# Kernel tuning notes

Measured on AMD Instinct MI355X. Metric: run time of the kernel, lower is better.

## Reference

```python
import jax, jax.numpy as jnp
import numpy as np

B, T, C = 4, 2048, 1024
N_HEAD = 16
HEAD_DIM = C // N_HEAD
SCALE = 1.0 / np.sqrt(HEAD_DIM).astype(np.float32)


def setup_inputs() -> dict:
    key = jax.random.key(0)
    k1, k2, k3 = jax.random.split(key, 3)
    x = jax.random.normal(k1, (B, T, C), dtype=jnp.float32)
    # torch Linear weights: [out_features, in_features], scaled init
    w_qkv = jax.random.normal(k2, (3 * C, C), dtype=jnp.float32) * (1.0 / np.sqrt(C))
    w_out = jax.random.normal(k3, (C, C), dtype=jnp.float32) * (1.0 / np.sqrt(C))
    b_out = jnp.zeros((C,), dtype=jnp.float32)
    return {"x": x, "w_qkv": w_qkv, "w_out": w_out, "b_out": b_out}


def reference(x, w_qkv, w_out, b_out):
    Bsz, Tlen, Cdim = x.shape
    qkv = jnp.einsum('btc,oc->bto', x, w_qkv)  # [B,T,3C]
    q, k, v = jnp.split(qkv, 3, axis=-1)
    # [B,H,T,D]
    def heads(t):
        return t.reshape(Bsz, Tlen, N_HEAD, HEAD_DIM).transpose(0, 2, 1, 3)
    q, k, v = heads(q), heads(k), heads(v)
    att = jnp.einsum('bhqd,bhkd->bhqk', q, k) * SCALE  # [B,H,T,T]
    causal = jnp.tril(jnp.ones((Tlen, Tlen), dtype=bool))
    att = jnp.where(causal[None, None], att, -jnp.inf)
    att = jax.nn.softmax(att, axis=-1)
    out = jnp.einsum('bhqk,bhkd->bhqd', att, v)
    out = out.transpose(0, 2, 1, 3).reshape(Bsz, Tlen, Cdim)
    out = jnp.einsum('btc,oc->bto', out, w_out) + b_out
    return out
```

## Files before the change

kernel.cpp:

```cpp
#include <hip/hip_runtime.h>
#include <stdint.h>


typedef __attribute__((ext_vector_type(8))) short bf16x8;
typedef __attribute__((ext_vector_type(4))) float f32x4;

#define EXP2F(x) __builtin_amdgcn_exp2f(x)
#define SL2E 0.18033688011112042f
#define FIXED_M 15.0f

template <bool B> struct BoolC { static constexpr bool value = B; };
template <int I> struct IntC { static constexpr int value = I; };

__device__ __forceinline__ short f2bf(float f) {
  union { float f; unsigned u; } c; c.f = f;
  unsigned u = c.u;
  unsigned r = (u + 0x7fffu + ((u >> 16) & 1u)) >> 16;
  return (short)(unsigned short)r;
}

__device__ __forceinline__ void softmax_pack(const f32x4* sc, bf16x8& pa0, bf16x8& pa1) {
  union U { int i[4]; bf16x8 v; };
  U u0, u1;
#pragma unroll
  for (int j = 0; j < 4; ++j) {
    float p0 = EXP2F(sc[j][0]);
    float p1 = EXP2F(sc[j][1]);
    float p2 = EXP2F(sc[j][2]);
    float p3 = EXP2F(sc[j][3]);
    int w0, w1;
    asm("v_cvt_pk_bf16_f32 %0, %1, %2" : "=v"(w0) : "v"(p0), "v"(p1));
    asm("v_cvt_pk_bf16_f32 %0, %1, %2" : "=v"(w1) : "v"(p2), "v"(p3));
    if (j < 2) { u0.i[j * 2] = w0; u0.i[j * 2 + 1] = w1; }
    else       { u1.i[(j - 2) * 2] = w0; u1.i[(j - 2) * 2 + 1] = w1; }
  }
  pa0 = u0.v;
  pa1 = u1.v;
}

__device__ __forceinline__ void llds16(const short* g, short* l) {
  __builtin_amdgcn_global_load_lds(
      (const __attribute__((address_space(1))) unsigned int*)g,
      (__attribute__((address_space(3))) unsigned int*)l, 16, 0, 0);
}

__global__ __launch_bounds__(256) void cast_all(
    const float* __restrict__ x, const float* __restrict__ wq,
    const float* __restrict__ wo, short* __restrict__ xb,
    short* __restrict__ wqb, short* __restrict__ wob) {
  const int b = blockIdx.x;
  const float* src;
  short* dst;
  int idx;
  if (b < 8192)        { src = x;  dst = xb;  idx = b * 256 + threadIdx.x; }
  else if (b < 11264)  { src = wq; dst = wqb; idx = (b - 8192) * 256 + threadIdx.x; }
  else                 { src = wo; dst = wob; idx = (b - 11264) * 256 + threadIdx.x; }
  float4 f = ((const float4*)src)[idx];
  short4 o;
  o.x = f2bf(f.x); o.y = f2bf(f.y); o.z = f2bf(f.z); o.w = f2bf(f.w);
  ((short4*)dst)[idx] = o;
}

__global__ __launch_bounds__(512) void gemm_qkv(
    const short* __restrict__ A, const short* __restrict__ Bw,
    short* __restrict__ Qo, short* __restrict__ Ko, short* __restrict__ Vt) {
  const int K = 1024;
  __shared__ short smem[49152];
  const int tid = threadIdx.x;
  const int lane = tid & 63;
  const int wave = tid >> 6;
  const int wr = wave >> 1;
  const int wc = wave & 1;
  const int m0 = blockIdx.y * 256;
  const int n0 = blockIdx.x * 128;
  const int mrow = lane & 15;
  const int kq = lane >> 4;

  f32x4 acc[4][4];
#pragma unroll
  for (int i = 0; i < 4; ++i)
#pragma unroll
    for (int j = 0; j < 4; ++j) acc[i][j] = (f32x4){0.f, 0.f, 0.f, 0.f};

  auto stageA = [&](int t, int buf, int ca) {
    const int c = ca * 512 + tid;
    const int row = c >> 3;
    const int sc = (c & 7) ^ (row & 7);
    llds16(A + (size_t)(m0 + row) * K + t * 64 + sc * 8,
           &smem[buf * 24576 + c * 8]);
  };
  auto stageB = [&](int t, int buf, int cb) {
    const int c = cb * 512 + tid;
    const int row = c >> 3;
    const int sc = (c & 7) ^ (row & 7);
    llds16(Bw + (size_t)(n0 + row) * K + t * 64 + sc * 8,
           &smem[buf * 24576 + 16384 + c * 8]);
  };

  auto rdA = [&](const short* lA, int i, int kk) -> bf16x8 {
    const int row = wr * 64 + i * 16 + mrow;
    const int ch = (kq + 4 * kk) ^ (row & 7);
    return *(const bf16x8*)&lA[row * 64 + ch * 8];
  };
  auto rdB = [&](const short* lB, int j, int kk) -> bf16x8 {
    const int row = wc * 64 + j * 16 + mrow;
    const int ch = (kq + 4 * kk) ^ (row & 7);
    return *(const bf16x8*)&lB[row * 64 + ch * 8];
  };

  stageA(0, 0, 0); stageA(0, 0, 1); stageA(0, 0, 2); stageA(0, 0, 3);
  stageB(0, 0, 0); stageB(0, 0, 1);
  asm volatile("s_waitcnt vmcnt(0)" ::: "memory");
  __syncthreads();

#define PHASE_TAIL()                                         \
  __builtin_amdgcn_s_barrier();                              \
  asm volatile("s_waitcnt lgkmcnt(0)" ::: "memory");         \
  __builtin_amdgcn_sched_barrier(0);                         \
  __builtin_amdgcn_s_setprio(1);

#define PHASE_END()                                          \
  __builtin_amdgcn_s_setprio(0);                             \
  __builtin_amdgcn_sched_barrier(0);                         \
  __builtin_amdgcn_s_barrier();

  for (int t = 0; t < 16; ++t) {
    const int buf = t & 1;
    const int nb = buf ^ 1;
    const short* lA = &smem[buf * 24576];
    const short* lB = lA + 16384;
    bf16x8 a0, a1, a2, a3, bf0, bf1, bf2, bf3;

    a0 = rdA(lA, 0, 0); a1 = rdA(lA, 1, 0);
    bf0 = rdB(lB, 0, 0); bf1 = rdB(lB, 1, 0);
    bf2 = rdB(lB, 2, 0); bf3 = rdB(lB, 3, 0);
    if (t < 15) { stageA(t + 1, nb, 0); stageA(t + 1, nb, 1); }
    PHASE_TAIL();
    acc[0][0] = __builtin_amdgcn_mfma_f32_16x16x32_bf16(a0, bf0, acc[0][0], 0, 0, 0);
    acc[0][1] = __builtin_amdgcn_mfma_f32_16x16x32_bf16(a0, bf1, acc[0][1], 0, 0, 0);
    acc[0][2] = __builtin_amdgcn_mfma_f32_16x16x32_bf16(a0, bf2, acc[0][2], 0, 0, 0);
    acc[0][3] = __builtin_amdgcn_mfma_f32_16x16x32_bf16(a0, bf3, acc[0][3], 0, 0, 0);
    acc[1][0] = __builtin_amdgcn_mfma_f32_16x16x32_bf16(a1, bf0, acc[1][0], 0, 0, 0);
    acc[1][1] = __builtin_amdgcn_mfma_f32_16x16x32_bf16(a1, bf1, acc[1][1], 0, 0, 0);
    acc[1][2] = __builtin_amdgcn_mfma_f32_16x16x32_bf16(a1, bf2, acc[1][2], 0, 0, 0);
    acc[1][3] = __builtin_amdgcn_mfma_f32_16x16x32_bf16(a1, bf3, acc[1][3], 0, 0, 0);
    PHASE_END();

    a2 = rdA(lA, 2, 0); a3 = rdA(lA, 3, 0);
    if (t < 15) { stageA(t + 1, nb, 2); stageA(t + 1, nb, 3); }
    PHASE_TAIL();
    acc[2][0] = __builtin_amdgcn_mfma_f32_16x16x32_bf16(a2, bf0, acc[2][0], 0, 0, 0);
    acc[2][1] = __builtin_amdgcn_mfma_f32_16x16x32_bf16(a2, bf1, acc[2][1], 0, 0, 0);
    acc[2][2] = __builtin_amdgcn_mfma_f32_16x16x32_bf16(a2, bf2, acc[2][2], 0, 0, 0);
    acc[2][3] = __builtin_amdgcn_mfma_f32_16x16x32_bf16(a2, bf3, acc[2][3], 0, 0, 0);
    acc[3][0] = __builtin_amdgcn_mfma_f32_16x16x32_bf16(a3, bf0, acc[3][0], 0, 0, 0);
    acc[3][1] = __builtin_amdgcn_mfma_f32_16x16x32_bf16(a3, bf1, acc[3][1], 0, 0, 0);
    acc[3][2] = __builtin_amdgcn_mfma_f32_16x16x32_bf16(a3, bf2, acc[3][2], 0, 0, 0);
    acc[3][3] = __builtin_amdgcn_mfma_f32_16x16x32_bf16(a3, bf3, acc[3][3], 0, 0, 0);
    PHASE_END();

    a0 = rdA(lA, 0, 1); a1 = rdA(lA, 1, 1);
    bf0 = rdB(lB, 0, 1); bf1 = rdB(lB, 1, 1);
    bf2 = rdB(lB, 2, 1); bf3 = rdB(lB, 3, 1);
    if (t < 15) { stageB(t + 1, nb, 0); stageB(t + 1, nb, 1); }
    PHASE_TAIL();
    acc[0][0] = __builtin_amdgcn_mfma_f32_16x16x32_bf16(a0, bf0, acc[0][0], 0, 0, 0);
    acc[0][1] = __builtin_amdgcn_mfma_f32_16x16x32_bf16(a0, bf1, acc[0][1], 0, 0, 0);
    acc[0][2] = __builtin_amdgcn_mfma_f32_16x16x32_bf16(a0, bf2, acc[0][2], 0, 0, 0);
    acc[0][3] = __builtin_amdgcn_mfma_f32_16x16x32_bf16(a0, bf3, acc[0][3], 0, 0, 0);
    acc[1][0] = __builtin_amdgcn_mfma_f32_16x16x32_bf16(a1, bf0, acc[1][0], 0, 0, 0);
    acc[1][1] = __builtin_amdgcn_mfma_f32_16x16x32_bf16(a1, bf1, acc[1][1], 0, 0, 0);
    acc[1][2] = __builtin_amdgcn_mfma_f32_16x16x32_bf16(a1, bf2, acc[1][2], 0, 0, 0);
    acc[1][3] = __builtin_amdgcn_mfma_f32_16x16x32_bf16(a1, bf3, acc[1][3], 0, 0, 0);
    PHASE_END();

    a2 = rdA(lA, 2, 1); a3 = rdA(lA, 3, 1);
    PHASE_TAIL();
    acc[2][0] = __builtin_amdgcn_mfma_f32_16x16x32_bf16(a2, bf0, acc[2][0], 0, 0, 0);
    acc[2][1] = __builtin_amdgcn_mfma_f32_16x16x32_bf16(a2, bf1, acc[2][1], 0, 0, 0);
    acc[2][2] = __builtin_amdgcn_mfma_f32_16x16x32_bf16(a2, bf2, acc[2][2], 0, 0, 0);
    acc[2][3] = __builtin_amdgcn_mfma_f32_16x16x32_bf16(a2, bf3, acc[2][3], 0, 0, 0);
    acc[3][0] = __builtin_amdgcn_mfma_f32_16x16x32_bf16(a3, bf0, acc[3][0], 0, 0, 0);
    acc[3][1] = __builtin_amdgcn_mfma_f32_16x16x32_bf16(a3, bf1, acc[3][1], 0, 0, 0);
    acc[3][2] = __builtin_amdgcn_mfma_f32_16x16x32_bf16(a3, bf2, acc[3][2], 0, 0, 0);
    acc[3][3] = __builtin_amdgcn_mfma_f32_16x16x32_bf16(a3, bf3, acc[3][3], 0, 0, 0);
    __builtin_amdgcn_s_setprio(0);
    __builtin_amdgcn_sched_barrier(0);
    if (t < 15) asm volatile("s_waitcnt vmcnt(0)" ::: "memory");
    __builtin_amdgcn_s_barrier();
  }
#undef PHASE_TAIL
#undef PHASE_END

  __syncthreads();

  const int b = m0 >> 11;
  if (n0 < 2048) {
    const float sc_ = ((n0 >> 10) == 1) ? SL2E : 1.0f;
    short* lC = smem;
#pragma unroll
    for (int i = 0; i < 4; ++i) {
      const int rl = wr * 64 + i * 16 + kq * 4;
#pragma unroll
      for (int j = 0; j < 4; ++j) {
        const int col = wc * 64 + j * 16 + mrow;
#pragma unroll
        for (int r = 0; r < 4; ++r)
          lC[(rl + r) * 132 + col] = f2bf(acc[i][j][r] * sc_);
      }
    }
    __syncthreads();
    short* dst = (n0 >> 10) == 0 ? Qo : Ko;
#pragma unroll
    for (int call = 0; call < 8; ++call) {
      const int cc = call * 512 + tid;
      const int row = cc >> 4;
      const int ch = cc & 15;
      const int t = (m0 & 2047) + row;
      const int c = (n0 + ch * 8) & 1023;
      const int h = c >> 6;
      const int d = c & 63;
      bf16x8 val = *(const bf16x8*)&lC[row * 132 + ch * 8];
      *(bf16x8*)(dst + ((size_t)(b * 16 + h) * 2048 + t) * 64 + d) = val;
    }
  } else {
    short* lCt = smem;
#pragma unroll
    for (int i = 0; i < 4; ++i) {
      const int rl = wr * 64 + i * 16 + kq * 4;
#pragma unroll
      for (int j = 0; j < 4; ++j) {
        const int col = wc * 64 + j * 16 + mrow;
#pragma unroll
        for (int r = 0; r < 4; ++r)
          lCt[col * 264 + rl + r] = f2bf(acc[i][j][r]);
      }
    }
    __syncthreads();
#pragma unroll
    for (int call = 0; call < 8; ++call) {
      const int cc = call * 512 + tid;
      const int col = cc >> 5;
      const int tg = cc & 31;
      const int o = n0 + col;
      const int d = o & 63;
      const int h = (o >> 6) & 15;
      const int t = (m0 & 2047) + tg * 8;
      bf16x8 val = *(const bf16x8*)&lCt[col * 264 + tg * 8];
      *(bf16x8*)(Vt + ((size_t)(b * 16 + h) * 64 + d) * 2048 + t) = val;
    }
  }
}

__global__ __launch_bounds__(256) void gemm_out(
    const short* __restrict__ A, const short* __restrict__ Bw,
    const float* __restrict__ bias, float* __restrict__ Out) {
  const int K = 1024;
  __shared__ short smem[16384];
  const int tid = threadIdx.x;
  const int lane = tid & 63;
  const int wave = tid >> 6;
  const int m0 = blockIdx.y * 128;
  const int n0 = blockIdx.x * 128;
  const int wm = (wave >> 1) * 64;
  const int wn = (wave & 1) * 64;
  const int mrow = lane & 15;
  const int kq = lane >> 4;

  f32x4 acc[4][4];
#pragma unroll
  for (int i = 0; i < 4; ++i)
#pragma unroll
    for (int j = 0; j < 4; ++j) acc[i][j] = (f32x4){0.f, 0.f, 0.f, 0.f};

  auto stage = [&](int it, int buf) {
#pragma unroll
    for (int call = 0; call < 2; ++call) {
      const int cb = call * 256 + wave * 64;
      const int c = cb + lane;
      const int row = c >> 2;
      const int scol = (c & 3) ^ ((row ^ (row >> 2)) & 3);
      llds16(A + (size_t)(m0 + row) * K + it * 32 + scol * 8,
             &smem[buf * 8192 + cb * 8]);
      llds16(Bw + (size_t)(n0 + row) * K + it * 32 + scol * 8,
             &smem[buf * 8192 + 4096 + cb * 8]);
    }
  };

  stage(0, 0);
  __syncthreads();

  for (int it = 0; it < 32; ++it) {
    const int buf = it & 1;
    if (it < 31) stage(it + 1, buf ^ 1);
    const short* lA = &smem[buf * 8192];
    const short* lB = &smem[buf * 8192 + 4096];
    bf16x8 af[4], bfr[4];
#pragma unroll
    for (int i = 0; i < 4; ++i) {
      const int row = wm + i * 16 + mrow;
      af[i] = *(const bf16x8*)&lA[row * 32 + (((kq ^ row ^ (row >> 2)) & 3) * 8)];
    }
#pragma unroll
    for (int j = 0; j < 4; ++j) {
      const int row = wn + j * 16 + mrow;
      bfr[j] = *(const bf16x8*)&lB[row * 32 + (((kq ^ row ^ (row >> 2)) & 3) * 8)];
    }
#pragma unroll
    for (int i = 0; i < 4; ++i)
#pragma unroll
      for (int j = 0; j < 4; ++j)
        acc[i][j] = __builtin_amdgcn_mfma_f32_16x16x32_bf16(af[i], bfr[j], acc[i][j], 0, 0, 0);
    __syncthreads();
  }

#pragma unroll
  for (int i = 0; i < 4; ++i) {
    const int m = m0 + wm + i * 16 + kq * 4;
#pragma unroll
    for (int j = 0; j < 4; ++j) {
      const int n = n0 + wn + j * 16 + mrow;
      const float bb = bias[n];
#pragma unroll
      for (int r = 0; r < 4; ++r)
        Out[(size_t)(m + r) * 1024 + n] = acc[i][j][r] + bb;
    }
  }
}

__global__ __launch_bounds__(256) void flash_attn(
    const short* __restrict__ Qg, const short* __restrict__ Kg,
    const short* __restrict__ Vtg, short* __restrict__ Og) {
  const int T = 2048;
  __shared__ short lK[2][64 * 64];
  __shared__ short lVt[2][64 * 64];
  const int tid = threadIdx.x;
  const int lane = tid & 63;
  const int wave = tid >> 6;
  const int bh = blockIdx.x;
  const int bx = blockIdx.y;
  const int mrow = lane & 15;
  const int kq = lane >> 4;
  const int swz = mrow & 7;
  const size_t base = (size_t)bh * T * 64;
  const size_t vbase = (size_t)bh * 64 * T;

  int qts[4];
  qts[0] = bx;
  qts[1] = 31 - bx;
  qts[2] = 15 - bx;
  qts[3] = 16 + bx;

  const bf16x8 ones = {0x3F80, 0x3F80, 0x3F80, 0x3F80, 0x3F80, 0x3F80, 0x3F80, 0x3F80};

  bf16x8 aq0[4], aq1[4];
#pragma unroll
  for (int s = 0; s < 4; ++s) {
    const short* qp = Qg + base + (size_t)(qts[s] * 64 + wave * 16 + mrow) * 64 + kq * 8;
    aq0[s] = *(const bf16x8*)qp;
    aq1[s] = *(const bf16x8*)(qp + 32);
  }

  f32x4 acc[4][4], lac[4];
#pragma unroll
  for (int s = 0; s < 4; ++s) {
    lac[s] = (f32x4){0.f, 0.f, 0.f, 0.f};
#pragma unroll
    for (int jd = 0; jd < 4; ++jd) acc[s][jd] = (f32x4){0.f, 0.f, 0.f, 0.f};
  }

  auto stage = [&](int nt, int buf) {
#pragma unroll
    for (int call = 0; call < 2; ++call) {
      const int cb = call * 256 + wave * 64;
      const int c = cb + lane;
      const int row = c >> 3;
      const int scol = (c & 7) ^ (row & 7);
      const int grow = (row & 0x23) | ((row & 0x0C) << 1) | ((row & 0x10) >> 2);
      llds16(Kg + base + (size_t)(nt * 64 + grow) * 64 + scol * 8, &lK[buf][cb * 8]);
      llds16(Vtg + vbase + (size_t)row * T + nt * 64 + scol * 8, &lVt[buf][cb * 8]);
    }
  };

  auto seg = [&](auto Aa, auto Pi, const short* K_, const short* Vt_, int kt) {
    constexpr bool ACT0 = decltype(Aa)::value;
    constexpr int pi = decltype(Pi)::value;
    f32x4 sc0[4], sc1[4];
#pragma unroll
    for (int j = 0; j < 4; ++j) {
      const short* krow = &K_[(j * 16 + mrow) * 64];
      bf16x8 kb0 = *(const bf16x8*)&krow[(kq ^ swz) * 8];
      bf16x8 kb1 = *(const bf16x8*)&krow[((4 + kq) ^ swz) * 8];
      __builtin_amdgcn_s_setprio(1);
      f32x4 ss = (f32x4){-FIXED_M, -FIXED_M, -FIXED_M, -FIXED_M};
      ss = __builtin_amdgcn_mfma_f32_16x16x32_bf16(kb0, aq0[pi + 1], ss, 0, 0, 0);
      ss = __builtin_amdgcn_mfma_f32_16x16x32_bf16(kb1, aq1[pi + 1], ss, 0, 0, 0);
      sc1[j] = ss;
      if constexpr (ACT0) {
        f32x4 s2 = (f32x4){-FIXED_M, -FIXED_M, -FIXED_M, -FIXED_M};
        s2 = __builtin_amdgcn_mfma_f32_16x16x32_bf16(kb0, aq0[pi], s2, 0, 0, 0);
        s2 = __builtin_amdgcn_mfma_f32_16x16x32_bf16(kb1, aq1[pi], s2, 0, 0, 0);
        sc0[j] = s2;
      }
      __builtin_amdgcn_s_setprio(0);
    }

    if (kt == qts[pi + 1]) {
      const int qcol = qts[pi + 1] * 64 + wave * 16 + mrow;
#pragma unroll
      for (int j = 0; j < 4; ++j) {
        const int keyb = kt * 64 + ((j & 2) << 4) + (kq << 3) + ((j & 1) << 2);
#pragma unroll
        for (int r = 0; r < 4; ++r)
          if (keyb + r > qcol) sc1[j][r] = -1e30f;
      }
    }
    if constexpr (ACT0) {
      if (kt == qts[pi]) {
        const int qcol = qts[pi] * 64 + wave * 16 + mrow;
#pragma unroll
        for (int j = 0; j < 4; ++j) {
          const int keyb = kt * 64 + ((j & 2) << 4) + (kq << 3) + ((j & 1) << 2);
#pragma unroll
          for (int r = 0; r < 4; ++r)
            if (keyb + r > qcol) sc0[j][r] = -1e30f;
        }
      }
    }

    bf16x8 pa0_1, pa1_1, pa0_0, pa1_0;
    softmax_pack(sc1, pa0_1, pa1_1);
    lac[pi + 1] = __builtin_amdgcn_mfma_f32_16x16x32_bf16(pa0_1, ones, lac[pi + 1], 0, 0, 0);
    lac[pi + 1] = __builtin_amdgcn_mfma_f32_16x16x32_bf16(pa1_1, ones, lac[pi + 1], 0, 0, 0);
    if constexpr (ACT0) {
      softmax_pack(sc0, pa0_0, pa1_0);
      lac[pi] = __builtin_amdgcn_mfma_f32_16x16x32_bf16(pa0_0, ones, lac[pi], 0, 0, 0);
      lac[pi] = __builtin_amdgcn_mfma_f32_16x16x32_bf16(pa1_0, ones, lac[pi], 0, 0, 0);
    }

#pragma unroll
    for (int jd = 0; jd < 4; ++jd) {
      const short* vrow = &Vt_[(jd * 16 + mrow) * 64];
      bf16x8 vb0 = *(const bf16x8*)&vrow[(kq ^ swz) * 8];
      bf16x8 vb1 = *(const bf16x8*)&vrow[((4 + kq) ^ swz) * 8];
      __builtin_amdgcn_s_setprio(1);
      acc[pi + 1][jd] = __builtin_amdgcn_mfma_f32_16x16x32_bf16(pa0_1, vb0, acc[pi + 1][jd], 0, 0, 0);
      acc[pi + 1][jd] = __builtin_amdgcn_mfma_f32_16x16x32_bf16(pa1_1, vb1, acc[pi + 1][jd], 0, 0, 0);
      if constexpr (ACT0) {
        acc[pi][jd] = __builtin_amdgcn_mfma_f32_16x16x32_bf16(pa0_0, vb0, acc[pi][jd], 0, 0, 0);
        acc[pi][jd] = __builtin_amdgcn_mfma_f32_16x16x32_bf16(pa1_0, vb1, acc[pi][jd], 0, 0, 0);
      }
      __builtin_amdgcn_s_setprio(0);
    }
  };

  stage(0, 0);
  const int ktmax = qts[1];
  for (int kt = 0; kt <= ktmax; ++kt) {
    const int bcur = kt & 1;
    if (kt < ktmax) {
      stage(kt + 1, bcur ^ 1);
      asm volatile("s_waitcnt vmcnt(4)" ::: "memory");
    } else {
      asm volatile("s_waitcnt vmcnt(0)" ::: "memory");
    }
    __builtin_amdgcn_s_barrier();
    const short* K_ = lK[bcur];
    const short* Vt_ = lVt[bcur];
    if (kt <= qts[0]) seg(BoolC<true>{}, IntC<0>{}, K_, Vt_, kt);
    else              seg(BoolC<false>{}, IntC<0>{}, K_, Vt_, kt);
    if (kt <= qts[3]) {
      if (kt <= qts[2]) seg(BoolC<true>{}, IntC<1 * 2>{}, K_, Vt_, kt);
      else              seg(BoolC<false>{}, IntC<1 * 2>{}, K_, Vt_, kt);
    }
    __builtin_amdgcn_s_barrier();
  }

  const int b = bh >> 4;
  const int h = bh & 15;
#pragma unroll
  for (int s = 0; s < 4; ++s) {
#pragma unroll
    for (int r = 0; r < 4; ++r) {
      const float inv = 1.0f / lac[s][r];
      const int t = qts[s] * 64 + wave * 16 + kq * 4 + r;
#pragma unroll
      for (int jd = 0; jd < 4; ++jd) {
        const int col = h * 64 + jd * 16 + mrow;
        Og[((size_t)b * 2048 + t) * 1024 + col] = f2bf(acc[s][jd][r] * inv);
      }
    }
  }
}

extern "C" void kernel_launch(void* const* d_in, const int* in_sizes, int n_in,
                              void* d_out, int out_size, void* d_ws, size_t ws_size,
                              hipStream_t stream) {
  const float* x = (const float*)d_in[0];
  const float* w_qkv = (const float*)d_in[1];
  const float* w_out = (const float*)d_in[2];
  const float* b_out = (const float*)d_in[3];
  float* out = (float*)d_out;

  char* ws = (char*)d_ws;
  const size_t NX = 8192ull * 1024;
  const size_t NWQ = 3072ull * 1024;
  const size_t NWO = 1024ull * 1024;
  const size_t NQ = 64ull * 2048 * 64;
  size_t off = 0;
  short* xb    = (short*)(ws + off); off += NX * 2;
  short* wqkvb = (short*)(ws + off); off += NWQ * 2;
  short* woutb = (short*)(ws + off); off += NWO * 2;
  short* q     = (short*)(ws + off); off += NQ * 2;
  short* k     = (short*)(ws + off); off += NQ * 2;
  short* vt    = (short*)(ws + off); off += NQ * 2;
  short* attb  = (short*)(ws + off); off += NX * 2;
  if (off > ws_size) return;

  cast_all<<<12288, 256, 0, stream>>>(x, w_qkv, w_out, xb, wqkvb, woutb);
  gemm_qkv<<<dim3(24, 32), 512, 0, stream>>>(xb, wqkvb, q, k, vt);
  flash_attn<<<dim3(64, 8), 256, 0, stream>>>(q, k, vt, attb);
  gemm_out<<<dim3(8, 64), 256, 0, stream>>>(attb, woutb, b_out, out);
}
```

Before: 248.2 us.

## Restructure output GEMM into 256x128 tiles with phased MFMA/load interleaving

The output projection GEMM now runs 512-thread blocks on 256x128 tiles with a K-step of 64. Each step splits into four phases that interleave LDS fragment reads, async global-to-LDS staging of the next tile, and MFMA bursts, with explicit barriers, waitcnts and setprio. The goal is to hide global load latency behind matrix math and get more reuse per tile. In exchange it uses more LDS (96KB) and more barriers per step, and halves the block count, which may hurt occupancy or tail balance.

```diff
diff --git a/kernel.cpp b/kernel.cpp
--- a/kernel.cpp
+++ b/kernel.cpp
@@ -252,18 +252,18 @@
   }
 }
 
-__global__ __launch_bounds__(256) void gemm_out(
+__global__ __launch_bounds__(512) void gemm_out(
     const short* __restrict__ A, const short* __restrict__ Bw,
     const float* __restrict__ bias, float* __restrict__ Out) {
   const int K = 1024;
-  __shared__ short smem[16384];
+  __shared__ short smem[49152];
   const int tid = threadIdx.x;
   const int lane = tid & 63;
   const int wave = tid >> 6;
-  const int m0 = blockIdx.y * 128;
+  const int wr = wave >> 1;
+  const int wc = wave & 1;
+  const int m0 = blockIdx.y * 256;
   const int n0 = blockIdx.x * 128;
-  const int wm = (wave >> 1) * 64;
-  const int wn = (wave & 1) * 64;
   const int mrow = lane & 15;
   const int kq = lane >> 4;
 
@@ -273,53 +273,122 @@
 #pragma unroll
     for (int j = 0; j < 4; ++j) acc[i][j] = (f32x4){0.f, 0.f, 0.f, 0.f};
 
-  auto stage = [&](int it, int buf) {
-#pragma unroll
-    for (int call = 0; call < 2; ++call) {
-      const int cb = call * 256 + wave * 64;
-      const int c = cb + lane;
-      const int row = c >> 2;
-      const int scol = (c & 3) ^ ((row ^ (row >> 2)) & 3);
-      llds16(A + (size_t)(m0 + row) * K + it * 32 + scol * 8,
-             &smem[buf * 8192 + cb * 8]);
-      llds16(Bw + (size_t)(n0 + row) * K + it * 32 + scol * 8,
-             &smem[buf * 8192 + 4096 + cb * 8]);
-    }
-  };
-
-  stage(0, 0);
+  auto stageA = [&](int t, int buf, int ca) {
+    const int c = ca * 512 + tid;
+    const int row = c >> 3;
+    const int sc = (c & 7) ^ (row & 7);
+    llds16(A + (size_t)(m0 + row) * K + t * 64 + sc * 8,
+           &smem[buf * 24576 + c * 8]);
+  };
+  auto stageB = [&](int t, int buf, int cb) {
+    const int c = cb * 512 + tid;
+    const int row = c >> 3;
+    const int sc = (c & 7) ^ (row & 7);
+    llds16(Bw + (size_t)(n0 + row) * K + t * 64 + sc * 8,
+           &smem[buf * 24576 + 16384 + c * 8]);
+  };
+
+  auto rdA = [&](const short* lA, int i, int kk) -> bf16x8 {
+    const int row = wr * 64 + i * 16 + mrow;
+    const int ch = (kq + 4 * kk) ^ (row & 7);
+    return *(const bf16x8*)&lA[row * 64 + ch * 8];
+  };
+  auto rdB = [&](const short* lB, int j, int kk) -> bf16x8 {
+    const int row = wc * 64 + j * 16 + mrow;
+    const int ch = (kq + 4 * kk) ^ (row & 7);
+    return *(const bf16x8*)&lB[row * 64 + ch * 8];
+  };
+
+  stageA(0, 0, 0); stageA(0, 0, 1); stageA(0, 0, 2); stageA(0, 0, 3);
+  stageB(0, 0, 0); stageB(0, 0, 1);
+  asm volatile("s_waitcnt vmcnt(0)" ::: "memory");
   __syncthreads();
 
-  for (int it = 0; it < 32; ++it) {
-    const int buf = it & 1;
-    if (it < 31) stage(it + 1, buf ^ 1);
-    const short* lA = &smem[buf * 8192];
-    const short* lB = &smem[buf * 8192 + 4096];
-    bf16x8 af[4], bfr[4];
-#pragma unroll
-    for (int i = 0; i < 4; ++i) {
-      const int row = wm + i * 16 + mrow;
-      af[i] = *(const bf16x8*)&lA[row * 32 + (((kq ^ row ^ (row >> 2)) & 3) * 8)];
-    }
+#define PHASE_TAIL()                                         \
+  __builtin_amdgcn_s_barrier();                              \
+  asm volatile("s_waitcnt lgkmcnt(0)" ::: "memory");         \
+  __builtin_amdgcn_sched_barrier(0);                         \
+  __builtin_amdgcn_s_setprio(1);
+
+#define PHASE_END()                                          \
+  __builtin_amdgcn_s_setprio(0);                             \
+  __builtin_amdgcn_sched_barrier(0);                         \
+  __builtin_amdgcn_s_barrier();
+
+  for (int t = 0; t < 16; ++t) {
+    const int buf = t & 1;
+    const int nb = buf ^ 1;
+    const short* lA = &smem[buf * 24576];
+    const short* lB = lA + 16384;
+    bf16x8 a0, a1, a2, a3, bf0, bf1, bf2, bf3;
+
+    a0 = rdA(lA, 0, 0); a1 = rdA(lA, 1, 0);
+    bf0 = rdB(lB, 0, 0); bf1 = rdB(lB, 1, 0);
+    bf2 = rdB(lB, 2, 0); bf3 = rdB(lB, 3, 0);
+    if (t < 15) { stageA(t + 1, nb, 0); stageA(t + 1, nb, 1); }
+    PHASE_TAIL();
+    acc[0][0] = __builtin_amdgcn_mfma_f32_16x16x32_bf16(a0, bf0, acc[0][0], 0, 0, 0);
+    acc[0][1] = __builtin_amdgcn_mfma_f32_16x16x32_bf16(a0, bf1, acc[0][1], 0, 0, 0);
+    acc[0][2] = __builtin_amdgcn_mfma_f32_16x16x32_bf16(a0, bf2, acc[0][2], 0, 0, 0);
+    acc[0][3] = __builtin_amdgcn_mfma_f32_16x16x32_bf16(a0, bf3, acc[0][3], 0, 0, 0);
+    acc[1][0] = __builtin_amdgcn_mfma_f32_16x16x32_bf16(a1, bf0, acc[1][0], 0, 0, 0);
+    acc[1][1] = __builtin_amdgcn_mfma_f32_16x16x32_bf16(a1, bf1, acc[1][1], 0, 0, 0);
+    acc[1][2] = __builtin_amdgcn_mfma_f32_16x16x32_bf16(a1, bf2, acc[1][2], 0, 0, 0);
+    acc[1][3] = __builtin_amdgcn_mfma_f32_16x16x32_bf16(a1, bf3, acc[1][3], 0, 0, 0);
+    PHASE_END();
+
+    a2 = rdA(lA, 2, 0); a3 = rdA(lA, 3, 0);
+    if (t < 15) { stageA(t + 1, nb, 2); stageA(t + 1, nb, 3); }
+    PHASE_TAIL();
+    acc[2][0] = __builtin_amdgcn_mfma_f32_16x16x32_bf16(a2, bf0, acc[2][0], 0, 0, 0);
+    acc[2][1] = __builtin_amdgcn_mfma_f32_16x16x32_bf16(a2, bf1, acc[2][1], 0, 0, 0);
+    acc[2][2] = __builtin_amdgcn_mfma_f32_16x16x32_bf16(a2, bf2, acc[2][2], 0, 0, 0);
+    acc[2][3] = __builtin_amdgcn_mfma_f32_16x16x32_bf16(a2, bf3, acc[2][3], 0, 0, 0);
+    acc[3][0] = __builtin_amdgcn_mfma_f32_16x16x32_bf16(a3, bf0, acc[3][0], 0, 0, 0);
+    acc[3][1] = __builtin_amdgcn_mfma_f32_16x16x32_bf16(a3, bf1, acc[3][1], 0, 0, 0);
+    acc[3][2] = __builtin_amdgcn_mfma_f32_16x16x32_bf16(a3, bf2, acc[3][2], 0, 0, 0);
+    acc[3][3] = __builtin_amdgcn_mfma_f32_16x16x32_bf16(a3, bf3, acc[3][3], 0, 0, 0);
+    PHASE_END();
+
+    a0 = rdA(lA, 0, 1); a1 = rdA(lA, 1, 1);
+    bf0 = rdB(lB, 0, 1); bf1 = rdB(lB, 1, 1);
+    bf2 = rdB(lB, 2, 1); bf3 = rdB(lB, 3, 1);
+    if (t < 15) { stageB(t + 1, nb, 0); stageB(t + 1, nb, 1); }
+    PHASE_TAIL();
+    acc[0][0] = __builtin_amdgcn_mfma_f32_16x16x32_bf16(a0, bf0, acc[0][0], 0, 0, 0);
+    acc[0][1] = __builtin_amdgcn_mfma_f32_16x16x32_bf16(a0, bf1, acc[0][1], 0, 0, 0);
+    acc[0][2] = __builtin_amdgcn_mfma_f32_16x16x32_bf16(a0, bf2, acc[0][2], 0, 0, 0);
+    acc[0][3] = __builtin_amdgcn_mfma_f32_16x16x32_bf16(a0, bf3, acc[0][3], 0, 0, 0);
+    acc[1][0] = __builtin_amdgcn_mfma_f32_16x16x32_bf16(a1, bf0, acc[1][0], 0, 0, 0);
+    acc[1][1] = __builtin_amdgcn_mfma_f32_16x16x32_bf16(a1, bf1, acc[1][1], 0, 0, 0);
+    acc[1][2] = __builtin_amdgcn_mfma_f32_16x16x32_bf16(a1, bf2, acc[1][2], 0, 0, 0);
+    acc[1][3] = __builtin_amdgcn_mfma_f32_16x16x32_bf16(a1, bf3, acc[1][3], 0, 0, 0);
+    PHASE_END();
+
+    a2 = rdA(lA, 2, 1); a3 = rdA(lA, 3, 1);
+    PHASE_TAIL();
+    acc[2][0] = __builtin_amdgcn_mfma_f32_16x16x32_bf16(a2, bf0, acc[2][0], 0, 0, 0);
+    acc[2][1] = __builtin_amdgcn_mfma_f32_16x16x32_bf16(a2, bf1, acc[2][1], 0, 0, 0);
+    acc[2][2] = __builtin_amdgcn_mfma_f32_16x16x32_bf16(a2, bf2, acc[2][2], 0, 0, 0);
+    acc[2][3] = __builtin_amdgcn_mfma_f32_16x16x32_bf16(a2, bf3, acc[2][3], 0, 0, 0);
+    acc[3][0] = __builtin_amdgcn_mfma_f32_16x16x32_bf16(a3, bf0, acc[3][0], 0, 0, 0);
+    acc[3][1] = __builtin_amdgcn_mfma_f32_16x16x32_bf16(a3, bf1, acc[3][1], 0, 0, 0);
+    acc[3][2] = __builtin_amdgcn_mfma_f32_16x16x32_bf16(a3, bf2, acc[3][2], 0, 0, 0);
+    acc[3][3] = __builtin_amdgcn_mfma_f32_16x16x32_bf16(a3, bf3, acc[3][3], 0, 0, 0);
+    __builtin_amdgcn_s_setprio(0);
+    __builtin_amdgcn_sched_barrier(0);
+    if (t < 15) asm volatile("s_waitcnt vmcnt(0)" ::: "memory");
+    __builtin_amdgcn_s_barrier();
+  }
+#undef PHASE_TAIL
+#undef PHASE_END
+
+#pragma unroll
+  for (int i = 0; i < 4; ++i) {
+    const int m = m0 + wr * 64 + i * 16 + kq * 4;
 #pragma unroll
     for (int j = 0; j < 4; ++j) {
-      const int row = wn + j * 16 + mrow;
-      bfr[j] = *(const bf16x8*)&lB[row * 32 + (((kq ^ row ^ (row >> 2)) & 3) * 8)];
-    }
-#pragma unroll
-    for (int i = 0; i < 4; ++i)
-#pragma unroll
-      for (int j = 0; j < 4; ++j)
-        acc[i][j] = __builtin_amdgcn_mfma_f32_16x16x32_bf16(af[i], bfr[j], acc[i][j], 0, 0, 0);
-    __syncthreads();
-  }
-
-#pragma unroll
-  for (int i = 0; i < 4; ++i) {
-    const int m = m0 + wm + i * 16 + kq * 4;
-#pragma unroll
-    for (int j = 0; j < 4; ++j) {
-      const int n = n0 + wn + j * 16 + mrow;
+      const int n = n0 + wc * 64 + j * 16 + mrow;
       const float bb = bias[n];
 #pragma unroll
       for (int r = 0; r < 4; ++r)
@@ -520,5 +589,5 @@
   cast_all<<<12288, 256, 0, stream>>>(x, w_qkv, w_out, xb, wqkvb, woutb);
   gemm_qkv<<<dim3(24, 32), 512, 0, stream>>>(xb, wqkvb, q, k, vt);
   flash_attn<<<dim3(64, 8), 256, 0, stream>>>(q, k, vt, attb);
-  gemm_out<<<dim3(8, 64), 256, 0, stream>>>(attb, woutb, b_out, out);
-}
+  gemm_out<<<dim3(8, 32), 512, 0, stream>>>(attb, woutb, b_out, out);
+}
```

New measurement: 242.8 us. 1.02x faster.
